# Performance work log

Measured on AMD Instinct MI355X. Metric: run time of the kernel, lower is better.

The kernel has to match this reference:

```python
import jax, jax.numpy as jnp
import numpy as np

NUM_CLASSES = 19
K = 100                 # max_views_per_class
TEMP = 0.1
BASE_TEMP = 0.07
EPS_NORM = 1e-12


def _l2_normalize(x):
    # matches torch F.normalize(dim=1): x / max(||x||, eps)
    n = jnp.sqrt(jnp.sum(x * x, axis=1, keepdims=True))
    return x / jnp.maximum(n, EPS_NORM)


def _sample_indices(labels_flat):
    # Deterministic per-class sampler: first K pixels of each class.
    # (torch version uses randperm; the downstream math is identical.)
    # Every class is guaranteed >= K pixels by input construction.
    idxs = [jnp.where(labels_flat == c, size=K, fill_value=0)[0]
            for c in range(NUM_CLASSES)]
    return jnp.concatenate(idxs)  # [NUM_CLASSES*K]


def setup_inputs() -> dict:
    key = jax.random.key(0)
    k1, k2, k3, k4 = jax.random.split(key, 4)
    pixel_feats = jax.random.normal(k1, (8, 256, 128, 128), dtype=jnp.float32)
    labels = jax.random.randint(k2, (8, 128, 128), 0, NUM_CLASSES).astype(jnp.int64)
    memory_feats = jax.random.normal(k3, (20000, 256), dtype=jnp.float32)
    memory_labels = jax.random.randint(k4, (20000,), 0, NUM_CLASSES).astype(jnp.int64)
    return {"pixel_feats": pixel_feats, "labels": labels,
            "memory_feats": memory_feats, "memory_labels": memory_labels}


def reference(pixel_feats, labels, memory_feats, memory_labels):
    B, D, H, W = pixel_feats.shape
    feats_flat = pixel_feats.transpose(0, 2, 3, 1).reshape(-1, D)   # [B*H*W, D]
    labels_flat = labels.reshape(-1)

    idx = _sample_indices(labels_flat)
    anchor_feats = feats_flat[idx]                                  # [Na, D]
    anchor_labels = jnp.repeat(jnp.arange(NUM_CLASSES), K)          # [Na]

    contrast_feats = jnp.concatenate([anchor_feats, memory_feats], axis=0)
    contrast_labels = jnp.concatenate([anchor_labels, memory_labels], axis=0)

    a = _l2_normalize(anchor_feats)
    c = _l2_normalize(contrast_feats)
    logits = jnp.einsum('nd,md->nm', a, c) / TEMP                   # [Na, Nc]

    Na, Nc = logits.shape
    mask = (anchor_labels[:, None] == contrast_labels[None, :]).astype(logits.dtype)
    # remove self-contrast (diagonal of the first Na contrast columns)
    rows = jnp.arange(Na)
    logits_mask = jnp.ones((Na, Nc), dtype=logits.dtype).at[rows, rows].set(0.0)
    mask = mask * logits_mask

    exp_logits = jnp.exp(logits) * logits_mask
    log_prob = logits - jnp.log(exp_logits.sum(axis=1, keepdims=True) + 1e-12)

    pos_count = mask.sum(axis=1)                                    # [Na]
    valid = pos_count > 0
    mean_log_prob_pos = (mask * log_prob).sum(axis=1) / jnp.maximum(pos_count, 1.0)
    n_valid = jnp.maximum(jnp.sum(valid).astype(logits.dtype), 1.0)
    loss = -(TEMP / BASE_TEMP) * (jnp.sum(jnp.where(valid, mean_log_prob_pos, 0.0)) / n_valid)
    return loss
```

## Files before the change

### kernel.cpp

```cpp
#include <hip/hip_runtime.h>
#include <hip/hip_bf16.h>
#include <math.h>

#define NCLS   19
#define KPC    100
#define NA     1900
#define NM     20000
#define NC     21900
#define NCP2   22016
#define D      256
#define HW     16384
#define NPIX   131072
#define NT_M   15
#define NT_N   172

typedef __attribute__((ext_vector_type(8))) short bf16x8;
typedef __attribute__((ext_vector_type(4))) float f32x4;

#define WS_IDX   0
#define WS_ROWS  7680
#define WS_ROWP  15360
#define WS_ROWC  23040
#define WS_CLAB  30720
#define WS_CT2   118784

__device__ __forceinline__ short f2bf(float x) {
    __hip_bfloat16 h = __float2bfloat16(x);
    return *(short*)&h;
}

__global__ void init_kernel(float* rowS, float* rowP, float* rowC, int* clab,
                            const int* __restrict__ memlab, short* __restrict__ Ct2) {
    const int i = blockIdx.x * 256 + threadIdx.x;
    if (i < NCP2) clab[i] = (i < NA) ? ((i * 5243) >> 19)
                                     : ((i < NC) ? memlab[i - NA] : -1);
    if (i < 1920) { rowS[i] = 0.f; rowP[i] = 0.f; rowC[i] = 0.f; }
    if (i < 32 * (NCP2 - NC)) {
        const int kq = i / (NCP2 - NC);
        const int n  = NC + i % (NCP2 - NC);
        bf16x8 z = {};
        *(bf16x8*)(Ct2 + ((size_t)kq * NCP2 + n) * 8) = z;
    }
}

__global__ void sample_kernel(const int* __restrict__ labels, int* __restrict__ idx) {
    const int c = blockIdx.x;
    const int t = threadIdx.x;
    const int wave = t >> 6, lane = t & 63;
    __shared__ int s_base;
    __shared__ int s_wavecnt[4];
    if (t == 0) s_base = 0;
    __syncthreads();
    for (int start = 0; start < NPIX; start += 256) {
        const int i = start + t;
        const bool pred = (labels[i] == c);
        const unsigned long long b = __ballot(pred);
        if (lane == 0) s_wavecnt[wave] = __popcll(b);
        __syncthreads();
        const int base = s_base;
        int wbase = 0;
        for (int w = 0; w < wave; ++w) wbase += s_wavecnt[w];
        const int chunk_total = s_wavecnt[0] + s_wavecnt[1] + s_wavecnt[2] + s_wavecnt[3];
        if (pred) {
            const int rank = base + wbase + __popcll(b & ((1ULL << lane) - 1ULL));
            if (rank < KPC) idx[c * KPC + rank] = i;
        }
        __syncthreads();
        if (t == 0) s_base = base + chunk_total;
        if (base + chunk_total >= KPC) break;
    }
}

__global__ void anchor_kernel(const float* __restrict__ pixel, const int* __restrict__ idx,
                              short* __restrict__ Ct2) {
    const int t = threadIdx.x;
    const int a = blockIdx.x * 8 + (t >> 5);
    const int kq = t & 31;
    if (a >= NA) return;
    const int p = idx[a];
    const int b = p >> 14;
    const int hw = p & (HW - 1);
    const float* base = pixel + ((size_t)(b * D + kq * 8)) * HW + hw;
    float v[8];
    float ssq = 0.f;
    #pragma unroll
    for (int j = 0; j < 8; ++j) { v[j] = base[(size_t)j * HW]; ssq += v[j] * v[j]; }
    #pragma unroll
    for (int o = 16; o; o >>= 1) ssq += __shfl_xor(ssq, o, 32);
    const float inv = 1.0f / fmaxf(sqrtf(ssq), 1e-12f);
    bf16x8 out;
    #pragma unroll
    for (int j = 0; j < 8; ++j) out[j] = f2bf(v[j] * inv);
    *(bf16x8*)(Ct2 + ((size_t)kq * NCP2 + a) * 8) = out;
}

__global__ void memory_kernel(const float* __restrict__ mem, short* __restrict__ Ct2) {
    const int t = threadIdx.x;
    const int r = blockIdx.x * 8 + (t >> 5);
    const int kq = t & 31;
    const float4 v0 = *(const float4*)(mem + (size_t)r * D + kq * 8);
    const float4 v1 = *(const float4*)(mem + (size_t)r * D + kq * 8 + 4);
    float ssq = v0.x*v0.x + v0.y*v0.y + v0.z*v0.z + v0.w*v0.w
              + v1.x*v1.x + v1.y*v1.y + v1.z*v1.z + v1.w*v1.w;
    #pragma unroll
    for (int o = 16; o; o >>= 1) ssq += __shfl_xor(ssq, o, 32);
    const float inv = 1.0f / fmaxf(sqrtf(ssq), 1e-12f);
    bf16x8 out;
    out[0] = f2bf(v0.x * inv); out[1] = f2bf(v0.y * inv);
    out[2] = f2bf(v0.z * inv); out[3] = f2bf(v0.w * inv);
    out[4] = f2bf(v1.x * inv); out[5] = f2bf(v1.y * inv);
    out[6] = f2bf(v1.z * inv); out[7] = f2bf(v1.w * inv);
    *(bf16x8*)(Ct2 + ((size_t)kq * NCP2 + NA + r) * 8) = out;
}

__global__ __launch_bounds__(256, 3)
void mfma_gemm_kernel(const short* __restrict__ Ct2, const int* __restrict__ clab,
                      float* __restrict__ rowS, float* __restrict__ rowP,
                      float* __restrict__ rowC) {
    __shared__ __align__(16) short As[8 * 128 * 8];
    __shared__ __align__(16) short Bs[8 * 128 * 8];
    const int tid  = threadIdx.x;
    const int lane = tid & 63;
    const int w    = tid >> 6;
    const int wm   = w >> 1, wn = w & 1;
    const int m0   = blockIdx.x * 128;
    const int n0   = blockIdx.y * 128;
    const int quad = lane >> 4;
    const int l16  = lane & 15;

    f32x4 acc[4][4] = {};

    for (int kc = 0; kc < 4; ++kc) {
        #pragma unroll
        for (int i = 0; i < 4; ++i) {
            const int bl = (w * 4 + i) * 64;
            const int kq = bl >> 7;
            const int ml = bl & 127;
            const size_t gA = ((size_t)(kc * 8 + kq) * NCP2 + m0 + ml + lane) * 8;
            __builtin_amdgcn_global_load_lds(
                (const __attribute__((address_space(1))) void*)(Ct2 + gA),
                (__attribute__((address_space(3))) void*)(As + (size_t)bl * 8 + lane * 8),
                16, 0, 0);
            const size_t gB = ((size_t)(kc * 8 + kq) * NCP2 + n0 + ml + lane) * 8;
            __builtin_amdgcn_global_load_lds(
                (const __attribute__((address_space(1))) void*)(Ct2 + gB),
                (__attribute__((address_space(3))) void*)(Bs + (size_t)bl * 8 + lane * 8),
                16, 0, 0);
        }
        __syncthreads();
        #pragma unroll
        for (int ks = 0; ks < 2; ++ks) {
            const int kqb = ks * 4 + quad;
            bf16x8 af[4], bfr[4];
            #pragma unroll
            for (int mi = 0; mi < 4; ++mi)
                af[mi] = *(const bf16x8*)(As + ((kqb * 128) + wm * 64 + mi * 16 + l16) * 8);
            #pragma unroll
            for (int ni = 0; ni < 4; ++ni)
                bfr[ni] = *(const bf16x8*)(Bs + ((kqb * 128) + wn * 64 + ni * 16 + l16) * 8);
            #pragma unroll
            for (int mi = 0; mi < 4; ++mi)
                #pragma unroll
                for (int ni = 0; ni < 4; ++ni)
                    acc[mi][ni] = __builtin_amdgcn_mfma_f32_16x16x32_bf16(
                        af[mi], bfr[ni], acc[mi][ni], 0, 0, 0);
        }
        __syncthreads();
    }

    int nIdx[4], nLab[4];
    #pragma unroll
    for (int ni = 0; ni < 4; ++ni) {
        const int n = n0 + wn * 64 + ni * 16 + l16;
        nIdx[ni] = n;
        nLab[ni] = (n < NC) ? clab[n] : -1;
    }
    #pragma unroll
    for (int mi = 0; mi < 4; ++mi) {
        #pragma unroll
        for (int r = 0; r < 4; ++r) {
            const int m = m0 + wm * 64 + mi * 16 + quad * 4 + r;
            const int mlab = (m * 5243) >> 19;
            float s = 0.f, p = 0.f, cnt = 0.f;
            #pragma unroll
            for (int ni = 0; ni < 4; ++ni) {
                const int n = nIdx[ni];
                if (n < NC && n != m) {
                    const float l = acc[mi][ni][r] * 10.0f;
                    s += __expf(l);
                    if (nLab[ni] == mlab) { p += l; cnt += 1.f; }
                }
            }
            for (int o = 1; o < 16; o <<= 1) {
                s   += __shfl_xor(s, o, 64);
                p   += __shfl_xor(p, o, 64);
                cnt += __shfl_xor(cnt, o, 64);
            }
            if (l16 == 0 && m < NA) {
                atomicAdd(&rowS[m], s);
                atomicAdd(&rowP[m], p);
                atomicAdd(&rowC[m], cnt);
            }
        }
    }
}

__global__ void finalize_kernel(const float* __restrict__ rowS, const float* __restrict__ rowP,
                                const float* __restrict__ rowC, float* __restrict__ out) {
    const int t = threadIdx.x;
    float sum = 0.f, nval = 0.f;
    for (int n = t; n < NA; n += 256) {
        const float cnt = rowC[n];
        const float logS = logf(rowS[n] + 1e-12f);
        const float mean = (rowP[n] - cnt * logS) / fmaxf(cnt, 1.0f);
        if (cnt > 0.f) { sum += mean; nval += 1.f; }
    }
    for (int o = 32; o; o >>= 1) {
        sum += __shfl_xor(sum, o, 64);
        nval += __shfl_xor(nval, o, 64);
    }
    __shared__ float rs[4], rn[4];
    if ((t & 63) == 0) { rs[t >> 6] = sum; rn[t >> 6] = nval; }
    __syncthreads();
    if (t == 0) {
        const float s = rs[0] + rs[1] + rs[2] + rs[3];
        const float nv = rn[0] + rn[1] + rn[2] + rn[3];
        out[0] = -(0.1f / 0.07f) * (s / fmaxf(nv, 1.f));
    }
}

extern "C" void kernel_launch(void* const* d_in, const int* in_sizes, int n_in,
                              void* d_out, int out_size, void* d_ws, size_t ws_size,
                              hipStream_t stream) {
    const float* pixel  = (const float*)d_in[0];
    const int*   labels = (const int*)d_in[1];
    const float* mem    = (const float*)d_in[2];
    const int*   memlab = (const int*)d_in[3];
    char* ws = (char*)d_ws;
    int*   idx  = (int*)(ws + WS_IDX);
    float* rowS = (float*)(ws + WS_ROWS);
    float* rowP = (float*)(ws + WS_ROWP);
    float* rowC = (float*)(ws + WS_ROWC);
    int*   clab = (int*)(ws + WS_CLAB);
    short* Ct2  = (short*)(ws + WS_CT2);
    float* out  = (float*)d_out;

    init_kernel<<<dim3(86), dim3(256), 0, stream>>>(rowS, rowP, rowC, clab, memlab, Ct2);
    sample_kernel<<<dim3(NCLS), dim3(256), 0, stream>>>(labels, idx);
    anchor_kernel<<<dim3(238), dim3(256), 0, stream>>>(pixel, idx, Ct2);
    memory_kernel<<<dim3(2500), dim3(256), 0, stream>>>(mem, Ct2);
    mfma_gemm_kernel<<<dim3(NT_M, NT_N), dim3(256), 0, stream>>>(Ct2, clab, rowS, rowP, rowC);
    finalize_kernel<<<dim3(1), dim3(256), 0, stream>>>(rowS, rowP, rowC, out);
}
```

Baseline: 262.0 us.

## Fuse prep kernels, loop N-tiles per GEMM block, and fold finalize into last block

Init, sampling and memory normalization are merged into a single prep kernel that dispatches on block index ranges. The GEMM grid is cut so each block walks four N-tiles, keeping per-row partial sums in registers and issuing fewer atomics. Positive counts now come from a memory-label histogram instead of per-tile counting. Finalize runs in the last GEMM block, picked with an atomic counter, which drops two launches but makes the tail serial inside one block.

```diff
diff --git a/kernel.cpp b/kernel.cpp
--- a/kernel.cpp
+++ b/kernel.cpp
@@ -13,14 +13,23 @@
 #define NPIX   131072
 #define NT_M   15
 #define NT_N   172
+#define NCHUNK 43
+#define GEMM_GRID (NT_M * NCHUNK)
+
+#define B_SAMPLE 0
+#define B_MEM    19
+#define B_CLAB   2519
+#define B_PAD    2605
+#define B_ZERO   2620
+#define K1_GRID  2621
 
 typedef __attribute__((ext_vector_type(8))) short bf16x8;
 typedef __attribute__((ext_vector_type(4))) float f32x4;
 
-#define WS_IDX   0
-#define WS_ROWS  7680
-#define WS_ROWP  15360
-#define WS_ROWC  23040
+#define WS_CTR   0
+#define WS_ROWS  64
+#define WS_ROWP  7744
+#define WS_IDX   15424
 #define WS_CLAB  30720
 #define WS_CT2   118784
 
@@ -29,45 +38,70 @@
     return *(short*)&h;
 }
 
-__global__ void init_kernel(float* rowS, float* rowP, float* rowC, int* clab,
-                            const int* __restrict__ memlab, short* __restrict__ Ct2) {
-    const int i = blockIdx.x * 256 + threadIdx.x;
-    if (i < NCP2) clab[i] = (i < NA) ? ((i * 5243) >> 19)
-                                     : ((i < NC) ? memlab[i - NA] : -1);
-    if (i < 1920) { rowS[i] = 0.f; rowP[i] = 0.f; rowC[i] = 0.f; }
-    if (i < 32 * (NCP2 - NC)) {
-        const int kq = i / (NCP2 - NC);
-        const int n  = NC + i % (NCP2 - NC);
-        bf16x8 z = {};
-        *(bf16x8*)(Ct2 + ((size_t)kq * NCP2 + n) * 8) = z;
-    }
-}
-
-__global__ void sample_kernel(const int* __restrict__ labels, int* __restrict__ idx) {
-    const int c = blockIdx.x;
+__global__ void prep_kernel(const int* __restrict__ labels, const float* __restrict__ mem,
+                            const int* __restrict__ memlab,
+                            int* __restrict__ idx, int* __restrict__ clab,
+                            short* __restrict__ Ct2,
+                            float* __restrict__ rowS, float* __restrict__ rowP,
+                            int* __restrict__ ctr) {
+    const int b = blockIdx.x;
     const int t = threadIdx.x;
-    const int wave = t >> 6, lane = t & 63;
-    __shared__ int s_base;
-    __shared__ int s_wavecnt[4];
-    if (t == 0) s_base = 0;
-    __syncthreads();
-    for (int start = 0; start < NPIX; start += 256) {
-        const int i = start + t;
-        const bool pred = (labels[i] == c);
-        const unsigned long long b = __ballot(pred);
-        if (lane == 0) s_wavecnt[wave] = __popcll(b);
+    if (b < B_MEM) {
+        const int c = b;
+        const int wave = t >> 6, lane = t & 63;
+        __shared__ int s_base;
+        __shared__ int s_wavecnt[4];
+        if (t == 0) s_base = 0;
         __syncthreads();
-        const int base = s_base;
-        int wbase = 0;
-        for (int w = 0; w < wave; ++w) wbase += s_wavecnt[w];
-        const int chunk_total = s_wavecnt[0] + s_wavecnt[1] + s_wavecnt[2] + s_wavecnt[3];
-        if (pred) {
-            const int rank = base + wbase + __popcll(b & ((1ULL << lane) - 1ULL));
-            if (rank < KPC) idx[c * KPC + rank] = i;
-        }
-        __syncthreads();
-        if (t == 0) s_base = base + chunk_total;
-        if (base + chunk_total >= KPC) break;
+        for (int start = 0; start < NPIX; start += 256) {
+            const int i = start + t;
+            const bool pred = (labels[i] == c);
+            const unsigned long long bm = __ballot(pred);
+            if (lane == 0) s_wavecnt[wave] = __popcll(bm);
+            __syncthreads();
+            const int base = s_base;
+            int wbase = 0;
+            for (int w = 0; w < wave; ++w) wbase += s_wavecnt[w];
+            const int chunk_total = s_wavecnt[0] + s_wavecnt[1] + s_wavecnt[2] + s_wavecnt[3];
+            if (pred) {
+                const int rank = base + wbase + __popcll(bm & ((1ULL << lane) - 1ULL));
+                if (rank < KPC) idx[c * KPC + rank] = i;
+            }
+            __syncthreads();
+            if (t == 0) s_base = base + chunk_total;
+            if (base + chunk_total >= KPC) break;
+        }
+    } else if (b < B_CLAB) {
+        const int r  = (b - B_MEM) * 8 + (t >> 5);
+        const int kq = t & 31;
+        const float4 v0 = *(const float4*)(mem + (size_t)r * D + kq * 8);
+        const float4 v1 = *(const float4*)(mem + (size_t)r * D + kq * 8 + 4);
+        float ssq = v0.x*v0.x + v0.y*v0.y + v0.z*v0.z + v0.w*v0.w
+                  + v1.x*v1.x + v1.y*v1.y + v1.z*v1.z + v1.w*v1.w;
+        #pragma unroll
+        for (int o = 16; o; o >>= 1) ssq += __shfl_xor(ssq, o, 32);
+        const float inv = 1.0f / fmaxf(sqrtf(ssq), 1e-12f);
+        bf16x8 ov;
+        ov[0] = f2bf(v0.x * inv); ov[1] = f2bf(v0.y * inv);
+        ov[2] = f2bf(v0.z * inv); ov[3] = f2bf(v0.w * inv);
+        ov[4] = f2bf(v1.x * inv); ov[5] = f2bf(v1.y * inv);
+        ov[6] = f2bf(v1.z * inv); ov[7] = f2bf(v1.w * inv);
+        *(bf16x8*)(Ct2 + ((size_t)kq * NCP2 + NA + r) * 8) = ov;
+    } else if (b < B_PAD) {
+        const int i = (b - B_CLAB) * 256 + t;
+        clab[i] = (i < NA) ? ((i * 5243) >> 19)
+                           : ((i < NC) ? memlab[i - NA] : -1);
+    } else if (b < B_ZERO) {
+        const int e = (b - B_PAD) * 256 + t;
+        if (e < 32 * (NCP2 - NC)) {
+            const int kq = e / (NCP2 - NC);
+            const int n  = NC + (e - kq * (NCP2 - NC));
+            bf16x8 z = {};
+            *(bf16x8*)(Ct2 + ((size_t)kq * NCP2 + n) * 8) = z;
+        }
+    } else {
+        for (int i = t; i < 1920; i += 256) { rowS[i] = 0.f; rowP[i] = 0.f; }
+        if (t == 0) ctr[0] = 0;
     }
 }
 
@@ -78,9 +112,9 @@
     const int kq = t & 31;
     if (a >= NA) return;
     const int p = idx[a];
-    const int b = p >> 14;
+    const int bi = p >> 14;
     const int hw = p & (HW - 1);
-    const float* base = pixel + ((size_t)(b * D + kq * 8)) * HW + hw;
+    const float* base = pixel + ((size_t)(bi * D + kq * 8)) * HW + hw;
     float v[8];
     float ssq = 0.f;
     #pragma unroll
@@ -88,142 +122,152 @@
     #pragma unroll
     for (int o = 16; o; o >>= 1) ssq += __shfl_xor(ssq, o, 32);
     const float inv = 1.0f / fmaxf(sqrtf(ssq), 1e-12f);
-    bf16x8 out;
-    #pragma unroll
-    for (int j = 0; j < 8; ++j) out[j] = f2bf(v[j] * inv);
-    *(bf16x8*)(Ct2 + ((size_t)kq * NCP2 + a) * 8) = out;
-}
-
-__global__ void memory_kernel(const float* __restrict__ mem, short* __restrict__ Ct2) {
-    const int t = threadIdx.x;
-    const int r = blockIdx.x * 8 + (t >> 5);
-    const int kq = t & 31;
-    const float4 v0 = *(const float4*)(mem + (size_t)r * D + kq * 8);
-    const float4 v1 = *(const float4*)(mem + (size_t)r * D + kq * 8 + 4);
-    float ssq = v0.x*v0.x + v0.y*v0.y + v0.z*v0.z + v0.w*v0.w
-              + v1.x*v1.x + v1.y*v1.y + v1.z*v1.z + v1.w*v1.w;
-    #pragma unroll
-    for (int o = 16; o; o >>= 1) ssq += __shfl_xor(ssq, o, 32);
-    const float inv = 1.0f / fmaxf(sqrtf(ssq), 1e-12f);
-    bf16x8 out;
-    out[0] = f2bf(v0.x * inv); out[1] = f2bf(v0.y * inv);
-    out[2] = f2bf(v0.z * inv); out[3] = f2bf(v0.w * inv);
-    out[4] = f2bf(v1.x * inv); out[5] = f2bf(v1.y * inv);
-    out[6] = f2bf(v1.z * inv); out[7] = f2bf(v1.w * inv);
-    *(bf16x8*)(Ct2 + ((size_t)kq * NCP2 + NA + r) * 8) = out;
+    bf16x8 ov;
+    #pragma unroll
+    for (int j = 0; j < 8; ++j) ov[j] = f2bf(v[j] * inv);
+    *(bf16x8*)(Ct2 + ((size_t)kq * NCP2 + a) * 8) = ov;
 }
 
 __global__ __launch_bounds__(256, 3)
 void mfma_gemm_kernel(const short* __restrict__ Ct2, const int* __restrict__ clab,
+                      const int* __restrict__ memlab,
                       float* __restrict__ rowS, float* __restrict__ rowP,
-                      float* __restrict__ rowC) {
+                      int* __restrict__ ctr, float* __restrict__ out) {
     __shared__ __align__(16) short As[8 * 128 * 8];
     __shared__ __align__(16) short Bs[8 * 128 * 8];
     const int tid  = threadIdx.x;
     const int lane = tid & 63;
     const int w    = tid >> 6;
     const int wm   = w >> 1, wn = w & 1;
-    const int m0   = blockIdx.x * 128;
-    const int n0   = blockIdx.y * 128;
+    const int m0   = (blockIdx.x % NT_M) * 128;
+    const int bn   = blockIdx.x / NT_M;
     const int quad = lane >> 4;
     const int l16  = lane & 15;
 
-    f32x4 acc[4][4] = {};
-
-    for (int kc = 0; kc < 4; ++kc) {
-        #pragma unroll
-        for (int i = 0; i < 4; ++i) {
-            const int bl = (w * 4 + i) * 64;
-            const int kq = bl >> 7;
-            const int ml = bl & 127;
-            const size_t gA = ((size_t)(kc * 8 + kq) * NCP2 + m0 + ml + lane) * 8;
-            __builtin_amdgcn_global_load_lds(
-                (const __attribute__((address_space(1))) void*)(Ct2 + gA),
-                (__attribute__((address_space(3))) void*)(As + (size_t)bl * 8 + lane * 8),
-                16, 0, 0);
-            const size_t gB = ((size_t)(kc * 8 + kq) * NCP2 + n0 + ml + lane) * 8;
-            __builtin_amdgcn_global_load_lds(
-                (const __attribute__((address_space(1))) void*)(Ct2 + gB),
-                (__attribute__((address_space(3))) void*)(Bs + (size_t)bl * 8 + lane * 8),
-                16, 0, 0);
-        }
-        __syncthreads();
-        #pragma unroll
-        for (int ks = 0; ks < 2; ++ks) {
-            const int kqb = ks * 4 + quad;
-            bf16x8 af[4], bfr[4];
+    float sAcc[4][4] = {};
+    float pAcc[4][4] = {};
+
+    for (int nt = 0; nt < 4; ++nt) {
+        const int n0 = (bn * 4 + nt) * 128;
+        f32x4 acc[4][4] = {};
+        for (int kc = 0; kc < 4; ++kc) {
             #pragma unroll
-            for (int mi = 0; mi < 4; ++mi)
-                af[mi] = *(const bf16x8*)(As + ((kqb * 128) + wm * 64 + mi * 16 + l16) * 8);
+            for (int i = 0; i < 4; ++i) {
+                const int bl = (w * 4 + i) * 64;
+                const int kq = bl >> 7;
+                const int ml = bl & 127;
+                const size_t gA = ((size_t)(kc * 8 + kq) * NCP2 + m0 + ml + lane) * 8;
+                __builtin_amdgcn_global_load_lds(
+                    (const __attribute__((address_space(1))) void*)(Ct2 + gA),
+                    (__attribute__((address_space(3))) void*)(As + (size_t)bl * 8 + lane * 8),
+                    16, 0, 0);
+                const size_t gB = ((size_t)(kc * 8 + kq) * NCP2 + n0 + ml + lane) * 8;
+                __builtin_amdgcn_global_load_lds(
+                    (const __attribute__((address_space(1))) void*)(Ct2 + gB),
+                    (__attribute__((address_space(3))) void*)(Bs + (size_t)bl * 8 + lane * 8),
+                    16, 0, 0);
+            }
+            __syncthreads();
             #pragma unroll
-            for (int ni = 0; ni < 4; ++ni)
-                bfr[ni] = *(const bf16x8*)(Bs + ((kqb * 128) + wn * 64 + ni * 16 + l16) * 8);
+            for (int ks = 0; ks < 2; ++ks) {
+                const int kqb = ks * 4 + quad;
+                bf16x8 af[4], bfr[4];
+                #pragma unroll
+                for (int mi = 0; mi < 4; ++mi)
+                    af[mi] = *(const bf16x8*)(As + ((kqb * 128) + wm * 64 + mi * 16 + l16) * 8);
+                #pragma unroll
+                for (int ni = 0; ni < 4; ++ni)
+                    bfr[ni] = *(const bf16x8*)(Bs + ((kqb * 128) + wn * 64 + ni * 16 + l16) * 8);
+                #pragma unroll
+                for (int mi = 0; mi < 4; ++mi)
+                    #pragma unroll
+                    for (int ni = 0; ni < 4; ++ni)
+                        acc[mi][ni] = __builtin_amdgcn_mfma_f32_16x16x32_bf16(
+                            af[mi], bfr[ni], acc[mi][ni], 0, 0, 0);
+            }
+            __syncthreads();
+        }
+
+        int nLab[4];
+        #pragma unroll
+        for (int ni = 0; ni < 4; ++ni) {
+            const int n = n0 + wn * 64 + ni * 16 + l16;
+            nLab[ni] = (n < NC) ? clab[n] : -1;
+        }
+        #pragma unroll
+        for (int mi = 0; mi < 4; ++mi) {
             #pragma unroll
-            for (int mi = 0; mi < 4; ++mi)
-                #pragma unroll
-                for (int ni = 0; ni < 4; ++ni)
-                    acc[mi][ni] = __builtin_amdgcn_mfma_f32_16x16x32_bf16(
-                        af[mi], bfr[ni], acc[mi][ni], 0, 0, 0);
-        }
-        __syncthreads();
-    }
-
-    int nIdx[4], nLab[4];
-    #pragma unroll
-    for (int ni = 0; ni < 4; ++ni) {
-        const int n = n0 + wn * 64 + ni * 16 + l16;
-        nIdx[ni] = n;
-        nLab[ni] = (n < NC) ? clab[n] : -1;
-    }
+            for (int r = 0; r < 4; ++r) {
+                const int m = m0 + wm * 64 + mi * 16 + quad * 4 + r;
+                const int mlab = (m * 5243) >> 19;
+                float s = 0.f, p = 0.f;
+                #pragma unroll
+                for (int ni = 0; ni < 4; ++ni) {
+                    const int n = n0 + wn * 64 + ni * 16 + l16;
+                    if (n < NC && n != m) {
+                        const float l = acc[mi][ni][r] * 10.0f;
+                        s += __expf(l);
+                        if (nLab[ni] == mlab) p += l;
+                    }
+                }
+                sAcc[mi][r] += s;
+                pAcc[mi][r] += p;
+            }
+        }
+    }
+
     #pragma unroll
     for (int mi = 0; mi < 4; ++mi) {
         #pragma unroll
         for (int r = 0; r < 4; ++r) {
+            float s = sAcc[mi][r], p = pAcc[mi][r];
+            for (int o = 1; o < 16; o <<= 1) {
+                s += __shfl_xor(s, o, 64);
+                p += __shfl_xor(p, o, 64);
+            }
             const int m = m0 + wm * 64 + mi * 16 + quad * 4 + r;
-            const int mlab = (m * 5243) >> 19;
-            float s = 0.f, p = 0.f, cnt = 0.f;
-            #pragma unroll
-            for (int ni = 0; ni < 4; ++ni) {
-                const int n = nIdx[ni];
-                if (n < NC && n != m) {
-                    const float l = acc[mi][ni][r] * 10.0f;
-                    s += __expf(l);
-                    if (nLab[ni] == mlab) { p += l; cnt += 1.f; }
-                }
-            }
-            for (int o = 1; o < 16; o <<= 1) {
-                s   += __shfl_xor(s, o, 64);
-                p   += __shfl_xor(p, o, 64);
-                cnt += __shfl_xor(cnt, o, 64);
-            }
             if (l16 == 0 && m < NA) {
                 atomicAdd(&rowS[m], s);
                 atomicAdd(&rowP[m], p);
-                atomicAdd(&rowC[m], cnt);
-            }
-        }
-    }
-}
-
-__global__ void finalize_kernel(const float* __restrict__ rowS, const float* __restrict__ rowP,
-                                const float* __restrict__ rowC, float* __restrict__ out) {
-    const int t = threadIdx.x;
+            }
+        }
+    }
+
+    __shared__ int s_last;
+    __shared__ int hist[NCLS];
+    __shared__ float rs[4], rn[4];
+    __syncthreads();
+    if (tid == 0) {
+        __threadfence();
+        const int old = atomicAdd(ctr, 1);
+        s_last = (old == GEMM_GRID - 1) ? 1 : 0;
+    }
+    __syncthreads();
+    if (!s_last) return;
+
+    __threadfence();
+    if (tid < NCLS) hist[tid] = 0;
+    __syncthreads();
+    for (int i = tid; i < NM; i += 256) atomicAdd(&hist[memlab[i]], 1);
+    __syncthreads();
+
     float sum = 0.f, nval = 0.f;
-    for (int n = t; n < NA; n += 256) {
-        const float cnt = rowC[n];
-        const float logS = logf(rowS[n] + 1e-12f);
-        const float mean = (rowP[n] - cnt * logS) / fmaxf(cnt, 1.0f);
+    for (int n = tid; n < NA; n += 256) {
+        const float cnt  = (float)(KPC - 1 + hist[(n * 5243) >> 19]);
+        const float S    = __hip_atomic_load(&rowS[n], __ATOMIC_RELAXED, __HIP_MEMORY_SCOPE_AGENT);
+        const float P    = __hip_atomic_load(&rowP[n], __ATOMIC_RELAXED, __HIP_MEMORY_SCOPE_AGENT);
+        const float logS = logf(S + 1e-12f);
+        const float mean = (P - cnt * logS) / fmaxf(cnt, 1.0f);
         if (cnt > 0.f) { sum += mean; nval += 1.f; }
     }
     for (int o = 32; o; o >>= 1) {
-        sum += __shfl_xor(sum, o, 64);
+        sum  += __shfl_xor(sum, o, 64);
         nval += __shfl_xor(nval, o, 64);
     }
-    __shared__ float rs[4], rn[4];
-    if ((t & 63) == 0) { rs[t >> 6] = sum; rn[t >> 6] = nval; }
-    __syncthreads();
-    if (t == 0) {
-        const float s = rs[0] + rs[1] + rs[2] + rs[3];
+    if ((tid & 63) == 0) { rs[tid >> 6] = sum; rn[tid >> 6] = nval; }
+    __syncthreads();
+    if (tid == 0) {
+        const float s  = rs[0] + rs[1] + rs[2] + rs[3];
         const float nv = rn[0] + rn[1] + rn[2] + rn[3];
         out[0] = -(0.1f / 0.07f) * (s / fmaxf(nv, 1.f));
     }
@@ -237,18 +281,17 @@
     const float* mem    = (const float*)d_in[2];
     const int*   memlab = (const int*)d_in[3];
     char* ws = (char*)d_ws;
-    int*   idx  = (int*)(ws + WS_IDX);
+    int*   ctr  = (int*)(ws + WS_CTR);
     float* rowS = (float*)(ws + WS_ROWS);
     float* rowP = (float*)(ws + WS_ROWP);
-    float* rowC = (float*)(ws + WS_ROWC);
+    int*   idx  = (int*)(ws + WS_IDX);
     int*   clab = (int*)(ws + WS_CLAB);
     short* Ct2  = (short*)(ws + WS_CT2);
     float* out  = (float*)d_out;
 
-    init_kernel<<<dim3(86), dim3(256), 0, stream>>>(rowS, rowP, rowC, clab, memlab, Ct2);
-    sample_kernel<<<dim3(NCLS), dim3(256), 0, stream>>>(labels, idx);
+    prep_kernel<<<dim3(K1_GRID), dim3(256), 0, stream>>>(
+        labels, mem, memlab, idx, clab, Ct2, rowS, rowP, ctr);
     anchor_kernel<<<dim3(238), dim3(256), 0, stream>>>(pixel, idx, Ct2);
-    memory_kernel<<<dim3(2500), dim3(256), 0, stream>>>(mem, Ct2);
-    mfma_gemm_kernel<<<dim3(NT_M, NT_N), dim3(256), 0, stream>>>(Ct2, clab, rowS, rowP, rowC);
-    finalize_kernel<<<dim3(1), dim3(256), 0, stream>>>(rowS, rowP, rowC, out);
-}
+    mfma_gemm_kernel<<<dim3(GEMM_GRID), dim3(256), 0, stream>>>(
+        Ct2, clab, memlab, rowS, rowP, ctr, out);
+}
```

Measured after the change: 296.3 us. +13.1%, slower.
